# Optimization experiments

Hardware: AMD Instinct MI355X
Metric: run time of the kernel (lower is better)

The kernel has to match this reference:

```python
import jax, jax.numpy as jnp
import numpy as np

SP_BETA = 1.0       # rendering_options.sp_beta
INF_DELTA = 1e10    # use_inf_depth=True -> last delta is 1e10
EPS = 1e-10


def setup_inputs() -> dict:
    key = jax.random.key(0)
    k1, k2, k3 = jax.random.split(key, 3)
    B, R, S, C = 8, 16384, 64, 3  # batch, rays, samples-per-ray, rgb channels
    colors = jax.random.normal(k1, (B, R, S, C), dtype=jnp.float32)
    densities = jax.random.normal(k2, (B, R, S, 1), dtype=jnp.float32)
    # depths must be sorted (increasing) along the sample dimension
    depths = jnp.sort(
        jax.random.uniform(k3, (B, R, S, 1), dtype=jnp.float32, minval=0.1, maxval=6.0),
        axis=2,
    )
    return {"colors": colors, "densities": densities, "depths": depths}


def reference(colors, densities, depths):
    # deltas between consecutive samples, last delta = 1e10 (infinite far plane)
    deltas = depths[:, :, 1:] - depths[:, :, :-1]                      # [B,R,S-1,1]
    deltas = jnp.concatenate(
        [deltas, jnp.full_like(deltas[:, :, :1], INF_DELTA)], axis=2)  # [B,R,S,1]

    # clamp_mode == 'softplus' with beta=1.0: softplus(x*beta)/beta
    dens = jax.nn.softplus(densities * SP_BETA) / SP_BETA              # [B,R,S,1]

    alphas = 1.0 - jnp.exp(-deltas * dens)                             # [B,R,S,1]

    # transmittance: cumulative product of (1-alpha), with leading ones
    trans = jnp.cumprod(1.0 - alphas + EPS, axis=2)                    # [B,R,S,1]
    trans = jnp.concatenate([jnp.ones_like(trans[:, :, :1]), trans], axis=2)  # [B,R,S+1,1]

    final_transmittance = trans[:, :, -1, 0]                           # [B,R]
    weights = alphas * trans[:, :, :-1]                                # [B,R,S,1]

    rgb_final = (weights * colors).sum(axis=2)                         # [B,R,C]
    depth = (weights * depths).sum(axis=2)                             # [B,R,1]
    return rgb_final, depth, weights, final_transmittance
```

## Files before the change

kernel.cpp:

```cpp
#include <hip/hip_runtime.h>

#define INF_DELTA 1e10f
#define RM_EPS 1e-10f
#define LOG2E 1.4426950408889634f

__global__ __launch_bounds__(256) void raymarch_kernel(
    const float* __restrict__ colors,
    const float* __restrict__ densities,
    const float* __restrict__ depths,
    float* __restrict__ rgb_out,
    float* __restrict__ depth_out,
    float* __restrict__ weights_out,
    float* __restrict__ trans_out,
    int n_rays)
{
    const int lane = threadIdx.x & 63;
    const int ray  = blockIdx.x * 4 + (threadIdx.x >> 6);
    if (ray >= n_rays) return;

    const long base = (long)ray * 64 + lane;

    const float d = depths[base];
    const float x = densities[base];
    const float* cptr = colors + (long)ray * 192 + lane * 3;
    const float c0 = cptr[0], c1 = cptr[1], c2 = cptr[2];

    const float d_next = __shfl_down(d, 1, 64);
    const float delta = (lane == 63) ? INF_DELTA : (d_next - d);

    const float q   = __builtin_amdgcn_exp2f(-__builtin_fabsf(x) * LOG2E);
    const float l2  = __builtin_amdgcn_logf(1.0f + q);
    const float sp2 = __builtin_fmaf(__builtin_fmaxf(x, 0.0f), LOG2E, l2);
    const float y   = __builtin_amdgcn_exp2f(-delta * sp2);

    const float alpha = 1.0f - y;
    const float t     = y + RM_EPS;

    float p = t;
    #pragma unroll
    for (int off = 1; off < 64; off <<= 1) {
        const float o = __shfl_up(p, off, 64);
        p *= (lane >= off) ? o : 1.0f;
    }
    float trans_excl = __shfl_up(p, 1, 64);
    if (lane == 0) trans_excl = 1.0f;

    const float w      = alpha * trans_excl;
    const float finalT = __shfl(p, 63, 64);

    weights_out[base] = w;

    float s0 = w * c0, s1 = w * c1, s2 = w * c2, s3 = w * d;
    #pragma unroll
    for (int off = 1; off <= 2; off <<= 1) {
        s0 += __shfl_xor(s0, off, 64);
        s1 += __shfl_xor(s1, off, 64);
        s2 += __shfl_xor(s2, off, 64);
        s3 += __shfl_xor(s3, off, 64);
    }
    const int sel = lane & 3;
    float v = (sel == 0) ? s0 : (sel == 1) ? s1 : (sel == 2) ? s2 : s3;
    #pragma unroll
    for (int off = 4; off < 64; off <<= 1) {
        v += __shfl_xor(v, off, 64);
    }

    if (lane < 3) {
        rgb_out[(long)ray * 3 + lane] = v;
    } else if (lane == 3) {
        depth_out[ray] = v;
    } else if (lane == 4) {
        trans_out[ray] = finalT;
    }
}

extern "C" void kernel_launch(void* const* d_in, const int* in_sizes, int n_in,
                              void* d_out, int out_size, void* d_ws, size_t ws_size,
                              hipStream_t stream) {
    const float* colors    = (const float*)d_in[0];
    const float* densities = (const float*)d_in[1];
    const float* depths    = (const float*)d_in[2];

    const int n_rays = in_sizes[1] / 64;

    float* out      = (float*)d_out;
    float* rgb      = out;
    float* depth_o  = rgb + (long)n_rays * 3;
    float* weights  = depth_o + n_rays;
    float* trans    = weights + (long)n_rays * 64;

    const int blocks = (n_rays + 3) / 4;
    raymarch_kernel<<<blocks, 256, 0, stream>>>(
        colors, densities, depths, rgb, depth_o, weights, trans, n_rays);
}
```

Baseline: 198.1 us.

## Process four samples per thread with float4 loads and 16-lane scans

Each thread now handles four consecutive samples, loading depths, densities and colors as float4 vectors and writing weights as float4. The transmittance product is computed serially inside the thread and then scanned across 16 lanes instead of 64. Each wavefront now covers four rays, and each block 16 rays. The aim is fewer, wider memory transactions and fewer cross-lane shuffles in what should be a bandwidth-bound kernel, at the cost of more registers per thread and fewer threads in flight.

After: 201.4 us. No clear change (+1.7%).

```diff
diff --git a/kernel.cpp b/kernel.cpp
--- a/kernel.cpp
+++ b/kernel.cpp
@@ -4,72 +4,93 @@
 #define RM_EPS 1e-10f
 #define LOG2E 1.4426950408889634f
 
+__device__ __forceinline__ float softplus_log2(float x) {
+    const float q  = __builtin_amdgcn_exp2f(-__builtin_fabsf(x) * LOG2E);
+    const float l2 = __builtin_amdgcn_logf(1.0f + q);
+    return __builtin_fmaf(__builtin_fmaxf(x, 0.0f), LOG2E, l2);
+}
+
 __global__ __launch_bounds__(256) void raymarch_kernel(
-    const float* __restrict__ colors,
-    const float* __restrict__ densities,
-    const float* __restrict__ depths,
+    const float4* __restrict__ colors4,
+    const float4* __restrict__ densities4,
+    const float4* __restrict__ depths4,
     float* __restrict__ rgb_out,
     float* __restrict__ depth_out,
-    float* __restrict__ weights_out,
+    float4* __restrict__ weights4,
     float* __restrict__ trans_out,
     int n_rays)
 {
     const int lane = threadIdx.x & 63;
-    const int ray  = blockIdx.x * 4 + (threadIdx.x >> 6);
+    const int sl   = lane & 15;
+    const int ray  = blockIdx.x * 16 + (((int)threadIdx.x >> 6) << 2) + (lane >> 4);
     if (ray >= n_rays) return;
 
-    const long base = (long)ray * 64 + lane;
+    const long vbase = (long)ray * 16 + sl;
 
-    const float d = depths[base];
-    const float x = densities[base];
-    const float* cptr = colors + (long)ray * 192 + lane * 3;
-    const float c0 = cptr[0], c1 = cptr[1], c2 = cptr[2];
+    const float4 d4 = depths4[vbase];
+    const float4 x4 = densities4[vbase];
+    const float4* cp = colors4 + (long)ray * 48 + sl * 3;
+    const float4 ca = cp[0], cb = cp[1], cc = cp[2];
 
-    const float d_next = __shfl_down(d, 1, 64);
-    const float delta = (lane == 63) ? INF_DELTA : (d_next - d);
+    const float dnext = __shfl_down(d4.x, 1, 64);
+    const float del0 = d4.y - d4.x;
+    const float del1 = d4.z - d4.y;
+    const float del2 = d4.w - d4.z;
+    const float del3 = (sl == 15) ? INF_DELTA : (dnext - d4.w);
 
-    const float q   = __builtin_amdgcn_exp2f(-__builtin_fabsf(x) * LOG2E);
-    const float l2  = __builtin_amdgcn_logf(1.0f + q);
-    const float sp2 = __builtin_fmaf(__builtin_fmaxf(x, 0.0f), LOG2E, l2);
-    const float y   = __builtin_amdgcn_exp2f(-delta * sp2);
+    const float y0 = __builtin_amdgcn_exp2f(-del0 * softplus_log2(x4.x));
+    const float y1 = __builtin_amdgcn_exp2f(-del1 * softplus_log2(x4.y));
+    const float y2 = __builtin_amdgcn_exp2f(-del2 * softplus_log2(x4.z));
+    const float y3 = __builtin_amdgcn_exp2f(-del3 * softplus_log2(x4.w));
 
-    const float alpha = 1.0f - y;
-    const float t     = y + RM_EPS;
+    const float t0 = y0 + RM_EPS, t1 = y1 + RM_EPS;
+    const float t2 = y2 + RM_EPS, t3 = y3 + RM_EPS;
 
-    float p = t;
+    const float p1 = t0, p2 = t0 * t1, p3 = p2 * t2;
+    const float ptot = p3 * t3;
+
+    float P = ptot;
     #pragma unroll
-    for (int off = 1; off < 64; off <<= 1) {
-        const float o = __shfl_up(p, off, 64);
-        p *= (lane >= off) ? o : 1.0f;
+    for (int off = 1; off < 16; off <<= 1) {
+        const float o = __shfl_up(P, off, 16);
+        P *= (sl >= off) ? o : 1.0f;
     }
-    float trans_excl = __shfl_up(p, 1, 64);
-    if (lane == 0) trans_excl = 1.0f;
+    float Pexcl = __shfl_up(P, 1, 16);
+    if (sl == 0) Pexcl = 1.0f;
+    const float finalT = __shfl(P, 15, 16);
 
-    const float w      = alpha * trans_excl;
-    const float finalT = __shfl(p, 63, 64);
+    const float w0 = (1.0f - y0) * Pexcl;
+    const float w1 = (1.0f - y1) * (Pexcl * p1);
+    const float w2 = (1.0f - y2) * (Pexcl * p2);
+    const float w3 = (1.0f - y3) * (Pexcl * p3);
 
-    weights_out[base] = w;
+    float4 wv; wv.x = w0; wv.y = w1; wv.z = w2; wv.w = w3;
+    weights4[vbase] = wv;
 
-    float s0 = w * c0, s1 = w * c1, s2 = w * c2, s3 = w * d;
+    float s0 = w0*ca.x + w1*ca.w + w2*cb.z + w3*cc.y;
+    float s1 = w0*ca.y + w1*cb.x + w2*cb.w + w3*cc.z;
+    float s2 = w0*ca.z + w1*cb.y + w2*cc.x + w3*cc.w;
+    float s3 = w0*d4.x + w1*d4.y + w2*d4.z + w3*d4.w;
+
     #pragma unroll
     for (int off = 1; off <= 2; off <<= 1) {
-        s0 += __shfl_xor(s0, off, 64);
-        s1 += __shfl_xor(s1, off, 64);
-        s2 += __shfl_xor(s2, off, 64);
-        s3 += __shfl_xor(s3, off, 64);
+        s0 += __shfl_xor(s0, off, 16);
+        s1 += __shfl_xor(s1, off, 16);
+        s2 += __shfl_xor(s2, off, 16);
+        s3 += __shfl_xor(s3, off, 16);
     }
-    const int sel = lane & 3;
+    const int sel = sl & 3;
     float v = (sel == 0) ? s0 : (sel == 1) ? s1 : (sel == 2) ? s2 : s3;
     #pragma unroll
-    for (int off = 4; off < 64; off <<= 1) {
-        v += __shfl_xor(v, off, 64);
+    for (int off = 4; off < 16; off <<= 1) {
+        v += __shfl_xor(v, off, 16);
     }
 
-    if (lane < 3) {
-        rgb_out[(long)ray * 3 + lane] = v;
-    } else if (lane == 3) {
+    if (sl < 3) {
+        rgb_out[(long)ray * 3 + sl] = v;
+    } else if (sl == 3) {
         depth_out[ray] = v;
-    } else if (lane == 4) {
+    } else if (sl == 4) {
         trans_out[ray] = finalT;
     }
 }
@@ -77,19 +98,19 @@
 extern "C" void kernel_launch(void* const* d_in, const int* in_sizes, int n_in,
                               void* d_out, int out_size, void* d_ws, size_t ws_size,
                               hipStream_t stream) {
-    const float* colors    = (const float*)d_in[0];
-    const float* densities = (const float*)d_in[1];
-    const float* depths    = (const float*)d_in[2];
+    const float4* colors4    = (const float4*)d_in[0];
+    const float4* densities4 = (const float4*)d_in[1];
+    const float4* depths4    = (const float4*)d_in[2];
 
     const int n_rays = in_sizes[1] / 64;
 
     float* out      = (float*)d_out;
     float* rgb      = out;
     float* depth_o  = rgb + (long)n_rays * 3;
-    float* weights  = depth_o + n_rays;
-    float* trans    = weights + (long)n_rays * 64;
+    float4* weights = (float4*)(depth_o + n_rays);
+    float* trans    = (float*)(weights + (long)n_rays * 16);
 
-    const int blocks = (n_rays + 3) / 4;
+    const int blocks = (n_rays + 15) / 16;
     raymarch_kernel<<<blocks, 256, 0, stream>>>(
-        colors, densities, depths, rgb, depth_o, weights, trans, n_rays);
+        colors4, densities4, depths4, rgb, depth_o, weights, trans, n_rays);
 }
```
